# Kernel tuning notes

Hardware: AMD Instinct MI355X
Metric: run time of the kernel (lower is better)

Reference implementation:

```python
import jax, jax.numpy as jnp
import numpy as np

N_NODES = 100000
N_EDGES = 1600000
D_FEAT = 128
N_CLASSES = 10


def setup_inputs() -> dict:
    key = jax.random.key(0)
    ks = jax.random.split(key, 9)
    x = jax.random.normal(ks[0], (N_NODES, D_FEAT), dtype=jnp.float32)
    edge_src = jax.random.randint(ks[1], (N_EDGES,), 0, N_NODES, dtype=jnp.int32)
    edge_dst = jax.random.randint(ks[2], (N_EDGES,), 0, N_NODES, dtype=jnp.int32)
    s = 1.0 / np.sqrt(D_FEAT)
    W1 = jax.random.normal(ks[3], (D_FEAT, D_FEAT), dtype=jnp.float32) * s
    b1 = jax.random.normal(ks[4], (D_FEAT,), dtype=jnp.float32) * s
    W2 = jax.random.normal(ks[5], (D_FEAT, D_FEAT), dtype=jnp.float32) * s
    b2 = jax.random.normal(ks[6], (D_FEAT,), dtype=jnp.float32) * s
    W3 = jax.random.normal(ks[7], (D_FEAT, N_CLASSES), dtype=jnp.float32) * s
    b3 = jax.random.normal(ks[8], (N_CLASSES,), dtype=jnp.float32) * s
    return {"x": x, "edge_src": edge_src, "edge_dst": edge_dst,
            "W1": W1, "b1": b1, "W2": W2, "b2": b2, "W3": W3, "b3": b3}


def _neighbor_mean(x, src, dst, n_nodes):
    # scatter-mean of neighbor features; isolated nodes keep their own feature
    msg_sum = jax.ops.segment_sum(x[src], dst, num_segments=n_nodes)  # [N, D]
    deg = jax.ops.segment_sum(jnp.ones(src.shape, x.dtype), dst, num_segments=n_nodes)  # [N]
    mean = msg_sum / jnp.maximum(deg, 1.0)[:, None]
    return jnp.where(deg[:, None] > 0, mean, x)


def reference(x, edge_src, edge_dst, W1, b1, W2, b2, W3, b3):
    n = x.shape[0]
    # layer 1: aggregate -> linear -> tanh
    h = jnp.tanh(_neighbor_mean(x, edge_src, edge_dst, n) @ W1 + b1)
    # layer 2: aggregate -> linear -> tanh
    h = jnp.tanh(_neighbor_mean(h, edge_src, edge_dst, n) @ W2 + b2)
    # final linear head (no aggregation, no activation)
    logits = h @ W3 + b3
    return logits
```

## Files before the change

### kernel.cpp

```cpp
#include <hip/hip_runtime.h>

#define DF 128
#define AST 136
#define EPB 4096

typedef float f32x4 __attribute__((ext_vector_type(4)));
typedef short bf16x8 __attribute__((ext_vector_type(8)));

__device__ __forceinline__ ushort f2bf(float f) {
  union { float f; uint u; } c; c.f = f;
  uint u = c.u;
  uint r = (u + 0x7fffu + ((u >> 16) & 1u)) >> 16;
  return (ushort)r;
}
__device__ __forceinline__ float bf_lo(uint v) { union { uint u; float f; } c; c.u = v << 16; return c.f; }
__device__ __forceinline__ float bf_hi(uint v) { union { uint u; float f; } c; c.u = v & 0xffff0000u; return c.f; }

__device__ __forceinline__ void addv8(float* acc, uint4 v) {
  acc[0] += bf_lo(v.x); acc[1] += bf_hi(v.x);
  acc[2] += bf_lo(v.y); acc[3] += bf_hi(v.y);
  acc[4] += bf_lo(v.z); acc[5] += bf_hi(v.z);
  acc[6] += bf_lo(v.w); acc[7] += bf_hi(v.w);
}

__global__ void prep_hist_kernel(const int* __restrict__ dst, int* __restrict__ histG,
                                 int E, int nbuck, int nblocks,
                                 const float* __restrict__ x, ushort* __restrict__ xb,
                                 const float* __restrict__ W1, ushort* __restrict__ Wt1,
                                 const float* __restrict__ W2, ushort* __restrict__ Wt2,
                                 const float* __restrict__ W3, ushort* __restrict__ W3t,
                                 ushort* __restrict__ xbN, ushort* __restrict__ bufBN, int n4) {
  __shared__ int lh[512];
  int tid = threadIdx.x;
  if ((int)blockIdx.x < nblocks) {
    int blk = blockIdx.x;
    for (int i = tid; i < nbuck; i += 256) lh[i] = 0;
    __syncthreads();
    int base = blk * EPB + tid * 4;
#pragma unroll
    for (int it = 0; it < EPB / 1024; ++it) {
      int e = base + it * 1024;
      if (e + 3 < E) {
        int4 d4 = *(const int4*)(dst + e);
        atomicAdd(&lh[d4.x >> 8], 1);
        atomicAdd(&lh[d4.y >> 8], 1);
        atomicAdd(&lh[d4.z >> 8], 1);
        atomicAdd(&lh[d4.w >> 8], 1);
      } else {
#pragma unroll
        for (int q = 0; q < 4; ++q) {
          int ee = e + q;
          if (ee < E) atomicAdd(&lh[dst[ee] >> 8], 1);
        }
      }
    }
    __syncthreads();
    for (int i = tid; i < nbuck; i += 256) histG[(size_t)i * nblocks + blk] = lh[i];
    return;
  }
  int i = ((int)blockIdx.x - nblocks) * 256 + tid;
  if (i < n4) {
    float4 v = ((const float4*)x)[i];
    ushort4 o; o.x = f2bf(v.x); o.y = f2bf(v.y); o.z = f2bf(v.z); o.w = f2bf(v.w);
    ((ushort4*)xb)[i] = o;
    return;
  }
  int j = i - n4;
  if (j < DF * DF) {
    int nr = j >> 7, k = j & 127;
    Wt1[j] = f2bf(W1[(size_t)k * DF + nr]);
    return;
  }
  j -= DF * DF;
  if (j < DF * DF) {
    int nr = j >> 7, k = j & 127;
    Wt2[j] = f2bf(W2[(size_t)k * DF + nr]);
    return;
  }
  j -= DF * DF;
  if (j < 16 * DF) {
    int nr = j >> 7, k = j & 127;
    W3t[j] = (nr < 10) ? f2bf(W3[(size_t)k * 10 + nr]) : (ushort)0;
    return;
  }
  j -= 16 * DF;
  if (j < 16) { ((uint4*)xbN)[j] = (uint4){0, 0, 0, 0}; return; }
  j -= 16;
  if (j < 16) { ((uint4*)bufBN)[j] = (uint4){0, 0, 0, 0}; }
}

__global__ void scan1_kernel(const int* __restrict__ cnt, int* __restrict__ excl,
                             int* __restrict__ bsums, int n) {
  __shared__ int wsum[4];
  int t = threadIdx.x;
  int base = blockIdx.x * 1024 + t * 4;
  int v[4]; int s = 0;
#pragma unroll
  for (int i = 0; i < 4; i++) { int d = (base + i < n) ? cnt[base + i] : 0; v[i] = s; s += d; }
  int lane = t & 63, w = t >> 6;
  int sc = s;
#pragma unroll
  for (int off = 1; off < 64; off <<= 1) { int o = __shfl_up(sc, off); if (lane >= off) sc += o; }
  if (lane == 63) wsum[w] = sc;
  __syncthreads();
  int woff = 0;
  for (int i = 0; i < w; i++) woff += wsum[i];
  int toff = woff + (sc - s);
#pragma unroll
  for (int i = 0; i < 4; i++) if (base + i < n) excl[base + i] = toff + v[i];
  if (t == 255) bsums[blockIdx.x] = woff + sc;
}

__device__ __forceinline__ void scan_bsums_lds(const int* __restrict__ bsums, int nb,
                                               int* sbs, int* wsum) {
  int t = threadIdx.x;
  int v0 = (2 * t < nb) ? bsums[2 * t] : 0;
  int v1 = (2 * t + 1 < nb) ? bsums[2 * t + 1] : 0;
  int s = v0 + v1;
  int lane = t & 63, w = t >> 6;
  int sc = s;
#pragma unroll
  for (int off = 1; off < 64; off <<= 1) { int o = __shfl_up(sc, off); if (lane >= off) sc += o; }
  if (lane == 63) wsum[w] = sc;
  __syncthreads();
  int woff = 0;
  for (int i = 0; i < w; i++) woff += wsum[i];
  int excl = woff + sc - s;
  sbs[2 * t] = excl;
  sbs[2 * t + 1] = excl + v0;
  __syncthreads();
}

__global__ void bucket_scatter_kernel(const int* __restrict__ src, const int* __restrict__ dst,
                                      const int* __restrict__ histE, const int* __restrict__ bsums,
                                      int nb, uint* __restrict__ eb, int E, int nbuck, int nblocks) {
  __shared__ int lc[512];
  __shared__ int sbs[512];
  __shared__ int wsum[4];
  int tid = threadIdx.x, blk = blockIdx.x;
  scan_bsums_lds(bsums, nb, sbs, wsum);
  for (int i = tid; i < nbuck; i += 256) {
    int idx = i * nblocks + blk;
    lc[i] = histE[idx] + sbs[idx >> 10];
  }
  __syncthreads();
  int base = blk * EPB + tid * 4;
#pragma unroll
  for (int it = 0; it < EPB / 1024; ++it) {
    int e = base + it * 1024;
    if (e + 3 < E) {
      int4 s4 = *(const int4*)(src + e);
      int4 d4 = *(const int4*)(dst + e);
      int p0 = atomicAdd(&lc[d4.x >> 8], 1);
      eb[p0] = (uint)s4.x | ((uint)(d4.x & 255) << 24);
      int p1 = atomicAdd(&lc[d4.y >> 8], 1);
      eb[p1] = (uint)s4.y | ((uint)(d4.y & 255) << 24);
      int p2 = atomicAdd(&lc[d4.z >> 8], 1);
      eb[p2] = (uint)s4.z | ((uint)(d4.z & 255) << 24);
      int p3 = atomicAdd(&lc[d4.w >> 8], 1);
      eb[p3] = (uint)s4.w | ((uint)(d4.w & 255) << 24);
    } else {
#pragma unroll
      for (int q = 0; q < 4; ++q) {
        int ee = e + q;
        if (ee < E) {
          int d = dst[ee];
          int pos = atomicAdd(&lc[d >> 8], 1);
          eb[pos] = (uint)src[ee] | ((uint)(d & 255) << 24);
        }
      }
    }
  }
}

__global__ void bucket_sort_kernel(const uint* __restrict__ eb,
                                   const int* __restrict__ histE, const int* __restrict__ bsums,
                                   int nb, int* __restrict__ rowptr, int* __restrict__ csr,
                                   int N, int E, int nbuck, int nblocks) {
  __shared__ int cnt[256];
  __shared__ int cursor[256];
  __shared__ int sbs[512];
  __shared__ int wsum[4];
  int tid = threadIdx.x, b = blockIdx.x;
  scan_bsums_lds(bsums, nb, sbs, wsum);
  int idx = b * nblocks;
  int beg = histE[idx] + sbs[idx >> 10];
  int end = E;
  if (b + 1 < nbuck) { int i2 = (b + 1) * nblocks; end = histE[i2] + sbs[i2 >> 10]; }
  cnt[tid] = 0;
  __syncthreads();
  for (int e = beg + tid; e < end; e += 256)
    atomicAdd(&cnt[eb[e] >> 24], 1);
  __syncthreads();
  int v = cnt[tid];
  int lane = tid & 63, w = tid >> 6;
  int sc = v;
#pragma unroll
  for (int off = 1; off < 64; off <<= 1) { int o = __shfl_up(sc, off); if (lane >= off) sc += o; }
  if (lane == 63) wsum[w] = sc;
  __syncthreads();
  int woff = 0;
  for (int i = 0; i < w; i++) woff += wsum[i];
  int excl = woff + sc - v;
  int node = (b << 8) + tid;
  if (node <= N) rowptr[node] = beg + excl;
  cursor[tid] = beg + excl;
  __syncthreads();
  for (int e = beg + tid; e < end; e += 256) {
    uint vv = eb[e];
    int pos = atomicAdd(&cursor[vv >> 24], 1);
    csr[pos] = (int)(vv & 0x00FFFFFFu);
  }
}

__global__ __launch_bounds__(256) void aggregate_kernel(
    const ushort* __restrict__ xb, const int* __restrict__ rowptr,
    const int* __restrict__ csr, ushort* __restrict__ out, int n) {
  int tid = threadIdx.x;
  int node = (blockIdx.x * 256 + tid) >> 4;
  if (node >= n) return;
  uint c16 = (uint)(tid & 15) * 16u;
  int beg = rowptr[node], end = rowptr[node + 1];
  const char* xbase = (const char*)xb;
  float acc[8];
#pragma unroll
  for (int i = 0; i < 8; i++) acc[i] = 0.f;

#pragma unroll 1
  for (int e = beg; e < end; e += 4) {
    int e1 = e + 1, e2 = e + 2, e3 = e + 3;
    uint r0 = (uint)csr[e];
    uint r1 = (e1 < end) ? (uint)csr[e1] : (uint)n;
    uint r2 = (e2 < end) ? (uint)csr[e2] : (uint)n;
    uint r3 = (e3 < end) ? (uint)csr[e3] : (uint)n;
    uint4 v0 = *(const uint4*)(xbase + (r0 * 256u + c16));
    uint4 v1 = *(const uint4*)(xbase + (r1 * 256u + c16));
    uint4 v2 = *(const uint4*)(xbase + (r2 * 256u + c16));
    uint4 v3 = *(const uint4*)(xbase + (r3 * 256u + c16));
    addv8(acc, v0);
    addv8(acc, v1);
    addv8(acc, v2);
    addv8(acc, v3);
  }

  int deg = end - beg;
  uint4 r;
  if (deg > 0) {
    float inv = 1.0f / (float)deg;
    r.x = (uint)f2bf(acc[0] * inv) | ((uint)f2bf(acc[1] * inv) << 16);
    r.y = (uint)f2bf(acc[2] * inv) | ((uint)f2bf(acc[3] * inv) << 16);
    r.z = (uint)f2bf(acc[4] * inv) | ((uint)f2bf(acc[5] * inv) << 16);
    r.w = (uint)f2bf(acc[6] * inv) | ((uint)f2bf(acc[7] * inv) << 16);
  } else {
    r = *(const uint4*)(xbase + ((uint)node * 256u + c16));
  }
  *(uint4*)((char*)out + ((uint)node * 256u + c16)) = r;
}

__global__ __launch_bounds__(256) void gemm_tanh_mfma(
    const ushort* __restrict__ A, const ushort* __restrict__ Wt,
    const float* __restrict__ bias, ushort* __restrict__ out, int n, int ntiles) {
  __shared__ ushort Ws[128 * AST];
  __shared__ float bs[128];
  int tid = threadIdx.x;

  for (int i = tid; i < 128 * 16; i += 256) {
    int r = i >> 4, c = i & 15;
    uint4 v = ((const uint4*)(Wt + r * DF))[c];
    *(uint4*)&Ws[r * AST + c * 8] = v;
  }
  if (tid < 128) bs[tid] = bias[tid];
  __syncthreads();

  int lane = tid & 63, w = tid >> 6;
  int wr = (w >> 1) * 32;
  int wc = (w & 1) * 64;
  int r16 = lane & 15, g8 = (lane >> 4) * 8;

  for (int tile = blockIdx.x; tile < ntiles; tile += gridDim.x) {
    int node0 = tile * 64;
    int ra = node0 + wr + r16;      if (ra >= n) ra = n - 1;
    int rb = node0 + wr + 16 + r16; if (rb >= n) rb = n - 1;
    const ushort* pa = A + (size_t)ra * DF + g8;
    const ushort* pb = A + (size_t)rb * DF + g8;

    f32x4 acc[2][4];
#pragma unroll
    for (int i = 0; i < 2; i++)
#pragma unroll
      for (int j = 0; j < 4; j++) acc[i][j] = (f32x4){0.f, 0.f, 0.f, 0.f};

#pragma unroll
    for (int ks = 0; ks < 4; ++ks) {
      bf16x8 a0 = *(const bf16x8*)(pa + ks * 32);
      bf16x8 a1 = *(const bf16x8*)(pb + ks * 32);
      int k0 = ks * 32 + g8;
#pragma unroll
      for (int j = 0; j < 4; j++) {
        bf16x8 b = *(const bf16x8*)&Ws[(wc + j * 16 + r16) * AST + k0];
        acc[0][j] = __builtin_amdgcn_mfma_f32_16x16x32_bf16(a0, b, acc[0][j], 0, 0, 0);
        acc[1][j] = __builtin_amdgcn_mfma_f32_16x16x32_bf16(a1, b, acc[1][j], 0, 0, 0);
      }
    }

#pragma unroll
    for (int mi = 0; mi < 2; mi++) {
#pragma unroll
      for (int j = 0; j < 4; j++) {
        int col = wc + j * 16 + r16;
        float bv = bs[col];
        int rowb = wr + mi * 16 + (lane >> 4) * 4;
#pragma unroll
        for (int q = 0; q < 4; q++) {
          int node = node0 + rowb + q;
          if (node < n) {
            float vv = tanhf(acc[mi][j][q] + bv);
            out[(size_t)node * DF + col] = f2bf(vv);
          }
        }
      }
    }
  }
}

__global__ __launch_bounds__(256) void gemm2_head_mfma(
    const ushort* __restrict__ A, const ushort* __restrict__ Wt,
    const float* __restrict__ bias, const ushort* __restrict__ W3t,
    const float* __restrict__ b3, float* __restrict__ out, int n, int ntiles) {
  __shared__ ushort Hs[64 * AST];
  __shared__ ushort Ws[128 * AST];
  __shared__ ushort W3s[16 * AST];
  __shared__ float bs[128];
  int tid = threadIdx.x;

  for (int i = tid; i < 128 * 16; i += 256) {
    int r = i >> 4, c = i & 15;
    uint4 v = ((const uint4*)(Wt + r * DF))[c];
    *(uint4*)&Ws[r * AST + c * 8] = v;
  }
  {
    int r = tid >> 4, c = tid & 15;
    uint4 v = ((const uint4*)(W3t + r * DF))[c];
    *(uint4*)&W3s[r * AST + c * 8] = v;
  }
  if (tid < 128) bs[tid] = bias[tid];
  __syncthreads();

  int lane = tid & 63, w = tid >> 6;
  int wr = (w >> 1) * 32, wc = (w & 1) * 64;
  int r16 = lane & 15, g8 = (lane >> 4) * 8;

  for (int tile = blockIdx.x; tile < ntiles; tile += gridDim.x) {
    int node0 = tile * 64;
    int ra = node0 + wr + r16;      if (ra >= n) ra = n - 1;
    int rb = node0 + wr + 16 + r16; if (rb >= n) rb = n - 1;
    const ushort* pa = A + (size_t)ra * DF + g8;
    const ushort* pb = A + (size_t)rb * DF + g8;

    f32x4 acc[2][4];
#pragma unroll
    for (int i = 0; i < 2; i++)
#pragma unroll
      for (int j = 0; j < 4; j++) acc[i][j] = (f32x4){0.f, 0.f, 0.f, 0.f};

#pragma unroll
    for (int ks = 0; ks < 4; ++ks) {
      bf16x8 a0 = *(const bf16x8*)(pa + ks * 32);
      bf16x8 a1 = *(const bf16x8*)(pb + ks * 32);
      int k0 = ks * 32 + g8;
#pragma unroll
      for (int j = 0; j < 4; ++j) {
        bf16x8 b = *(const bf16x8*)&Ws[(wc + j * 16 + r16) * AST + k0];
        acc[0][j] = __builtin_amdgcn_mfma_f32_16x16x32_bf16(a0, b, acc[0][j], 0, 0, 0);
        acc[1][j] = __builtin_amdgcn_mfma_f32_16x16x32_bf16(a1, b, acc[1][j], 0, 0, 0);
      }
    }

    __syncthreads();
#pragma unroll
    for (int mi = 0; mi < 2; mi++) {
#pragma unroll
      for (int j = 0; j < 4; j++) {
        int col = wc + j * 16 + r16;
        float bv = bs[col];
        int rowb = wr + mi * 16 + (lane >> 4) * 4;
#pragma unroll
        for (int q = 0; q < 4; q++)
          Hs[(rowb + q) * AST + col] = f2bf(tanhf(acc[mi][j][q] + bv));
      }
    }
    __syncthreads();

    f32x4 h = (f32x4){0.f, 0.f, 0.f, 0.f};
#pragma unroll
    for (int ks = 0; ks < 4; ++ks) {
      int k0 = ks * 32 + g8;
      bf16x8 a = *(const bf16x8*)&Hs[(w * 16 + r16) * AST + k0];
      bf16x8 b = *(const bf16x8*)&W3s[r16 * AST + k0];
      h = __builtin_amdgcn_mfma_f32_16x16x32_bf16(a, b, h, 0, 0, 0);
    }
    if (r16 < 10) {
      float bv = b3[r16];
      int rowb = w * 16 + (lane >> 4) * 4;
#pragma unroll
      for (int q = 0; q < 4; q++) {
        int node = node0 + rowb + q;
        if (node < n) out[(size_t)node * 10 + r16] = h[q] + bv;
      }
    }
  }
}

extern "C" void kernel_launch(void* const* d_in, const int* in_sizes, int n_in,
                              void* d_out, int out_size, void* d_ws, size_t ws_size,
                              hipStream_t stream) {
  const float* x    = (const float*)d_in[0];
  const int*   esrc = (const int*)d_in[1];
  const int*   edst = (const int*)d_in[2];
  const float* W1   = (const float*)d_in[3];
  const float* b1   = (const float*)d_in[4];
  const float* W2   = (const float*)d_in[5];
  const float* b2   = (const float*)d_in[6];
  const float* W3   = (const float*)d_in[7];
  const float* b3   = (const float*)d_in[8];
  float* out = (float*)d_out;

  const int N = in_sizes[0] / DF;
  const int E = in_sizes[1];

  const int nbuck   = (N + 255) >> 8;
  const int nblocks = (E + EPB - 1) / EPB;
  const int M = nbuck * nblocks;

  char* ws = (char*)d_ws;
  int*  rowptr = (int*)ws;
  int*  csr    = rowptr + (N + 1);
  int*  histG  = csr + E;
  int*  histE  = histG + M;
  int*  bsums2 = histE + M;
  uint* eb     = (uint*)(bsums2 + 1024);
  size_t off = (size_t)((char*)(eb + E) - ws);
  off = (off + 255) & ~(size_t)255;
  ushort* xb  = (ushort*)(ws + off);     off += (size_t)(N + 1) * DF * 2; off = (off + 255) & ~(size_t)255;
  ushort* Wt1 = (ushort*)(ws + off);     off += (size_t)DF * DF * 2;
  ushort* Wt2 = (ushort*)(ws + off);     off += (size_t)DF * DF * 2;
  ushort* W3t = (ushort*)(ws + off);     off += (size_t)16 * DF * 2; off = (off + 255) & ~(size_t)255;
  ushort* bufA = (ushort*)(ws + off);    off += (size_t)N * DF * 2; off = (off + 255) & ~(size_t)255;
  ushort* bufB = (ushort*)(ws + off);

  int n4 = N * DF / 4;
  int prep_total = n4 + 2 * DF * DF + 16 * DF + 32;
  int prep_blocks = (prep_total + 255) / 256;
  prep_hist_kernel<<<nblocks + prep_blocks, 256, 0, stream>>>(
      edst, histG, E, nbuck, nblocks,
      x, xb, W1, Wt1, W2, Wt2, W3, W3t,
      xb + (size_t)N * DF, bufB + (size_t)N * DF, n4);

  int nb_m = (M + 1023) / 1024;
  scan1_kernel<<<nb_m, 256, 0, stream>>>(histG, histE, bsums2, M);
  bucket_scatter_kernel<<<nblocks, 256, 0, stream>>>(esrc, edst, histE, bsums2, nb_m, eb, E, nbuck, nblocks);
  bucket_sort_kernel<<<nbuck, 256, 0, stream>>>(eb, histE, bsums2, nb_m, rowptr, csr, N, E, nbuck, nblocks);

  int agg_blocks = (N + 15) / 16;
  int ntiles = (N + 63) / 64;
  int gemm_grid = ntiles < 512 ? ntiles : 512;

  aggregate_kernel<<<agg_blocks, 256, 0, stream>>>(xb, rowptr, csr, bufA, N);
  gemm_tanh_mfma<<<gemm_grid, 256, 0, stream>>>(bufA, Wt1, b1, bufB, N, ntiles);
  aggregate_kernel<<<agg_blocks, 256, 0, stream>>>(bufB, rowptr, csr, bufA, N);
  gemm2_head_mfma<<<gemm_grid, 256, 0, stream>>>(bufA, Wt2, b2, W3t, b3, out, N, ntiles);
}
```

Before: 204.4 us.

## Apply weights before aggregation, overlap first GEMM with scan, fuse head

The code uses linearity to swap the order of mean-aggregation and the linear layer, since mean(x)@W equals mean(x@W). That lets the first GEMM run on the raw features, so it is folded into the scan kernel and overlaps with CSR construction. Bias and tanh now run in the aggregation kernels, and the 10-class head is computed in the second aggregation using shuffle reductions. This removes one GEMM epilogue pass and the separate head kernel. In exchange, the bf16 rounding now happens at a different point, and head arithmetic moves from MFMA to scalar FMAs.

Measured after the change: 197.4 us. -3.4%, faster.

```diff
diff --git a/kernel.cpp b/kernel.cpp
--- a/kernel.cpp
+++ b/kernel.cpp
@@ -28,8 +28,7 @@
                                  const float* __restrict__ x, ushort* __restrict__ xb,
                                  const float* __restrict__ W1, ushort* __restrict__ Wt1,
                                  const float* __restrict__ W2, ushort* __restrict__ Wt2,
-                                 const float* __restrict__ W3, ushort* __restrict__ W3t,
-                                 ushort* __restrict__ xbN, ushort* __restrict__ bufBN, int n4) {
+                                 ushort* __restrict__ zbN, ushort* __restrict__ ybN, int n4) {
   __shared__ int lh[512];
   int tid = threadIdx.x;
   if ((int)blockIdx.x < nblocks) {
@@ -78,37 +77,107 @@
     return;
   }
   j -= DF * DF;
-  if (j < 16 * DF) {
-    int nr = j >> 7, k = j & 127;
-    W3t[j] = (nr < 10) ? f2bf(W3[(size_t)k * 10 + nr]) : (ushort)0;
-    return;
-  }
-  j -= 16 * DF;
-  if (j < 16) { ((uint4*)xbN)[j] = (uint4){0, 0, 0, 0}; return; }
+  if (j < 16) { ((uint4*)zbN)[j] = (uint4){0, 0, 0, 0}; return; }
   j -= 16;
-  if (j < 16) { ((uint4*)bufBN)[j] = (uint4){0, 0, 0, 0}; }
-}
-
-__global__ void scan1_kernel(const int* __restrict__ cnt, int* __restrict__ excl,
-                             int* __restrict__ bsums, int n) {
+  if (j < 16) { ((uint4*)ybN)[j] = (uint4){0, 0, 0, 0}; }
+}
+
+__device__ __forceinline__ void gemm_tiles(const ushort* __restrict__ A,
+                                           const ushort* __restrict__ Ws,
+                                           ushort* __restrict__ out, int n, int ntiles,
+                                           int tile0, int tstride, int tid) {
+  int lane = tid & 63, w = tid >> 6;
+  int wr = (w >> 1) * 32, wc = (w & 1) * 64;
+  int r16 = lane & 15, g8 = (lane >> 4) * 8;
+  for (int tile = tile0; tile < ntiles; tile += tstride) {
+    int node0 = tile * 64;
+    int ra = node0 + wr + r16;      if (ra >= n) ra = n - 1;
+    int rb = node0 + wr + 16 + r16; if (rb >= n) rb = n - 1;
+    const ushort* pa = A + (size_t)ra * DF + g8;
+    const ushort* pb = A + (size_t)rb * DF + g8;
+
+    f32x4 acc[2][4];
+#pragma unroll
+    for (int i = 0; i < 2; i++)
+#pragma unroll
+      for (int j = 0; j < 4; j++) acc[i][j] = (f32x4){0.f, 0.f, 0.f, 0.f};
+
+#pragma unroll
+    for (int ks = 0; ks < 4; ++ks) {
+      bf16x8 a0 = *(const bf16x8*)(pa + ks * 32);
+      bf16x8 a1 = *(const bf16x8*)(pb + ks * 32);
+      int k0 = ks * 32 + g8;
+#pragma unroll
+      for (int j = 0; j < 4; j++) {
+        bf16x8 b = *(const bf16x8*)&Ws[(wc + j * 16 + r16) * AST + k0];
+        acc[0][j] = __builtin_amdgcn_mfma_f32_16x16x32_bf16(a0, b, acc[0][j], 0, 0, 0);
+        acc[1][j] = __builtin_amdgcn_mfma_f32_16x16x32_bf16(a1, b, acc[1][j], 0, 0, 0);
+      }
+    }
+
+#pragma unroll
+    for (int mi = 0; mi < 2; mi++) {
+#pragma unroll
+      for (int j = 0; j < 4; j++) {
+        int col = wc + j * 16 + r16;
+        int rowb = wr + mi * 16 + (lane >> 4) * 4;
+#pragma unroll
+        for (int q = 0; q < 4; q++) {
+          int node = node0 + rowb + q;
+          if (node < n) out[(size_t)node * DF + col] = f2bf(acc[mi][j][q]);
+        }
+      }
+    }
+  }
+}
+
+__global__ __launch_bounds__(256) void scan1_gemm_kernel(
+    const int* __restrict__ cnt, int* __restrict__ excl, int* __restrict__ bsums, int Mn,
+    int nb_m, const ushort* __restrict__ xb, const ushort* __restrict__ Wt1,
+    ushort* __restrict__ yb, int n, int ntiles) {
+  __shared__ ushort Ws[128 * AST];
   __shared__ int wsum[4];
   int t = threadIdx.x;
-  int base = blockIdx.x * 1024 + t * 4;
-  int v[4]; int s = 0;
-#pragma unroll
-  for (int i = 0; i < 4; i++) { int d = (base + i < n) ? cnt[base + i] : 0; v[i] = s; s += d; }
-  int lane = t & 63, w = t >> 6;
-  int sc = s;
-#pragma unroll
-  for (int off = 1; off < 64; off <<= 1) { int o = __shfl_up(sc, off); if (lane >= off) sc += o; }
-  if (lane == 63) wsum[w] = sc;
-  __syncthreads();
-  int woff = 0;
-  for (int i = 0; i < w; i++) woff += wsum[i];
-  int toff = woff + (sc - s);
-#pragma unroll
-  for (int i = 0; i < 4; i++) if (base + i < n) excl[base + i] = toff + v[i];
-  if (t == 255) bsums[blockIdx.x] = woff + sc;
+  if ((int)blockIdx.x < nb_m) {
+    int base = blockIdx.x * 1024 + t * 4;
+    int v[4]; int s = 0;
+#pragma unroll
+    for (int i = 0; i < 4; i++) { int d = (base + i < Mn) ? cnt[base + i] : 0; v[i] = s; s += d; }
+    int lane = t & 63, w = t >> 6;
+    int sc = s;
+#pragma unroll
+    for (int off = 1; off < 64; off <<= 1) { int o = __shfl_up(sc, off); if (lane >= off) sc += o; }
+    if (lane == 63) wsum[w] = sc;
+    __syncthreads();
+    int woff = 0;
+    for (int i = 0; i < w; i++) woff += wsum[i];
+    int toff = woff + (sc - s);
+#pragma unroll
+    for (int i = 0; i < 4; i++) if (base + i < Mn) excl[base + i] = toff + v[i];
+    if (t == 255) bsums[blockIdx.x] = woff + sc;
+    return;
+  }
+  for (int i = t; i < 128 * 16; i += 256) {
+    int r = i >> 4, c = i & 15;
+    uint4 v = ((const uint4*)(Wt1 + r * DF))[c];
+    *(uint4*)&Ws[r * AST + c * 8] = v;
+  }
+  __syncthreads();
+  gemm_tiles(xb, Ws, yb, n, ntiles, (int)blockIdx.x - nb_m, (int)gridDim.x - nb_m, t);
+}
+
+__global__ __launch_bounds__(256) void gemm_plain_kernel(
+    const ushort* __restrict__ A, const ushort* __restrict__ Wt,
+    ushort* __restrict__ out, int n, int ntiles) {
+  __shared__ ushort Ws[128 * AST];
+  int t = threadIdx.x;
+  for (int i = t; i < 128 * 16; i += 256) {
+    int r = i >> 4, c = i & 15;
+    uint4 v = ((const uint4*)(Wt + r * DF))[c];
+    *(uint4*)&Ws[r * AST + c * 8] = v;
+  }
+  __syncthreads();
+  gemm_tiles(A, Ws, out, n, ntiles, blockIdx.x, gridDim.x, t);
 }
 
 __device__ __forceinline__ void scan_bsums_lds(const int* __restrict__ bsums, int nb,
@@ -213,202 +282,111 @@
   }
 }
 
-__global__ __launch_bounds__(256) void aggregate_kernel(
-    const ushort* __restrict__ xb, const int* __restrict__ rowptr,
-    const int* __restrict__ csr, ushort* __restrict__ out, int n) {
+__device__ __forceinline__ void gather_mean(const ushort* __restrict__ src,
+                                            const int* __restrict__ rowptr,
+                                            const int* __restrict__ csr,
+                                            int node, int n, uint c16, float* acc) {
+  int beg = rowptr[node], end = rowptr[node + 1];
+  const char* xbase = (const char*)src;
+#pragma unroll
+  for (int i = 0; i < 8; i++) acc[i] = 0.f;
+  int deg = end - beg;
+  if (deg > 0) {
+#pragma unroll 1
+    for (int e = beg; e < end; e += 4) {
+      int e1 = e + 1, e2 = e + 2, e3 = e + 3;
+      uint r0 = (uint)csr[e];
+      uint r1 = (e1 < end) ? (uint)csr[e1] : (uint)n;
+      uint r2 = (e2 < end) ? (uint)csr[e2] : (uint)n;
+      uint r3 = (e3 < end) ? (uint)csr[e3] : (uint)n;
+      uint4 v0 = *(const uint4*)(xbase + (r0 * 256u + c16));
+      uint4 v1 = *(const uint4*)(xbase + (r1 * 256u + c16));
+      uint4 v2 = *(const uint4*)(xbase + (r2 * 256u + c16));
+      uint4 v3 = *(const uint4*)(xbase + (r3 * 256u + c16));
+      addv8(acc, v0);
+      addv8(acc, v1);
+      addv8(acc, v2);
+      addv8(acc, v3);
+    }
+    float inv = 1.0f / (float)deg;
+#pragma unroll
+    for (int i = 0; i < 8; i++) acc[i] *= inv;
+  } else {
+    uint4 v = *(const uint4*)(xbase + ((uint)node * 256u + c16));
+    float t[8] = {0, 0, 0, 0, 0, 0, 0, 0};
+    addv8(t, v);
+#pragma unroll
+    for (int i = 0; i < 8; i++) acc[i] = t[i];
+  }
+}
+
+__global__ __launch_bounds__(256) void agg_bias_tanh_kernel(
+    const ushort* __restrict__ yb, const int* __restrict__ rowptr,
+    const int* __restrict__ csr, const float* __restrict__ bias,
+    ushort* __restrict__ h1, int n) {
   int tid = threadIdx.x;
   int node = (blockIdx.x * 256 + tid) >> 4;
   if (node >= n) return;
   uint c16 = (uint)(tid & 15) * 16u;
-  int beg = rowptr[node], end = rowptr[node + 1];
-  const char* xbase = (const char*)xb;
   float acc[8];
-#pragma unroll
-  for (int i = 0; i < 8; i++) acc[i] = 0.f;
-
-#pragma unroll 1
-  for (int e = beg; e < end; e += 4) {
-    int e1 = e + 1, e2 = e + 2, e3 = e + 3;
-    uint r0 = (uint)csr[e];
-    uint r1 = (e1 < end) ? (uint)csr[e1] : (uint)n;
-    uint r2 = (e2 < end) ? (uint)csr[e2] : (uint)n;
-    uint r3 = (e3 < end) ? (uint)csr[e3] : (uint)n;
-    uint4 v0 = *(const uint4*)(xbase + (r0 * 256u + c16));
-    uint4 v1 = *(const uint4*)(xbase + (r1 * 256u + c16));
-    uint4 v2 = *(const uint4*)(xbase + (r2 * 256u + c16));
-    uint4 v3 = *(const uint4*)(xbase + (r3 * 256u + c16));
-    addv8(acc, v0);
-    addv8(acc, v1);
-    addv8(acc, v2);
-    addv8(acc, v3);
-  }
-
-  int deg = end - beg;
+  gather_mean(yb, rowptr, csr, node, n, c16, acc);
+  int d8 = (tid & 15) * 8;
+  float4 bA = *(const float4*)(bias + d8);
+  float4 bB = *(const float4*)(bias + d8 + 4);
+  float h0 = tanhf(acc[0] + bA.x), hh1 = tanhf(acc[1] + bA.y);
+  float h2 = tanhf(acc[2] + bA.z), h3 = tanhf(acc[3] + bA.w);
+  float h4 = tanhf(acc[4] + bB.x), h5 = tanhf(acc[5] + bB.y);
+  float h6 = tanhf(acc[6] + bB.z), h7 = tanhf(acc[7] + bB.w);
   uint4 r;
-  if (deg > 0) {
-    float inv = 1.0f / (float)deg;
-    r.x = (uint)f2bf(acc[0] * inv) | ((uint)f2bf(acc[1] * inv) << 16);
-    r.y = (uint)f2bf(acc[2] * inv) | ((uint)f2bf(acc[3] * inv) << 16);
-    r.z = (uint)f2bf(acc[4] * inv) | ((uint)f2bf(acc[5] * inv) << 16);
-    r.w = (uint)f2bf(acc[6] * inv) | ((uint)f2bf(acc[7] * inv) << 16);
-  } else {
-    r = *(const uint4*)(xbase + ((uint)node * 256u + c16));
-  }
-  *(uint4*)((char*)out + ((uint)node * 256u + c16)) = r;
-}
-
-__global__ __launch_bounds__(256) void gemm_tanh_mfma(
-    const ushort* __restrict__ A, const ushort* __restrict__ Wt,
-    const float* __restrict__ bias, ushort* __restrict__ out, int n, int ntiles) {
-  __shared__ ushort Ws[128 * AST];
-  __shared__ float bs[128];
+  r.x = (uint)f2bf(h0) | ((uint)f2bf(hh1) << 16);
+  r.y = (uint)f2bf(h2) | ((uint)f2bf(h3) << 16);
+  r.z = (uint)f2bf(h4) | ((uint)f2bf(h5) << 16);
+  r.w = (uint)f2bf(h6) | ((uint)f2bf(h7) << 16);
+  *(uint4*)((char*)h1 + ((uint)node * 256u + c16)) = r;
+}
+
+__global__ __launch_bounds__(256) void agg_head_kernel(
+    const ushort* __restrict__ zb, const int* __restrict__ rowptr,
+    const int* __restrict__ csr, const float* __restrict__ b2,
+    const float* __restrict__ W3, const float* __restrict__ b3,
+    float* __restrict__ out, int n) {
+  __shared__ float W3s[DF * 10];
   int tid = threadIdx.x;
-
-  for (int i = tid; i < 128 * 16; i += 256) {
-    int r = i >> 4, c = i & 15;
-    uint4 v = ((const uint4*)(Wt + r * DF))[c];
-    *(uint4*)&Ws[r * AST + c * 8] = v;
-  }
-  if (tid < 128) bs[tid] = bias[tid];
-  __syncthreads();
-
-  int lane = tid & 63, w = tid >> 6;
-  int wr = (w >> 1) * 32;
-  int wc = (w & 1) * 64;
-  int r16 = lane & 15, g8 = (lane >> 4) * 8;
-
-  for (int tile = blockIdx.x; tile < ntiles; tile += gridDim.x) {
-    int node0 = tile * 64;
-    int ra = node0 + wr + r16;      if (ra >= n) ra = n - 1;
-    int rb = node0 + wr + 16 + r16; if (rb >= n) rb = n - 1;
-    const ushort* pa = A + (size_t)ra * DF + g8;
-    const ushort* pb = A + (size_t)rb * DF + g8;
-
-    f32x4 acc[2][4];
-#pragma unroll
-    for (int i = 0; i < 2; i++)
-#pragma unroll
-      for (int j = 0; j < 4; j++) acc[i][j] = (f32x4){0.f, 0.f, 0.f, 0.f};
-
-#pragma unroll
-    for (int ks = 0; ks < 4; ++ks) {
-      bf16x8 a0 = *(const bf16x8*)(pa + ks * 32);
-      bf16x8 a1 = *(const bf16x8*)(pb + ks * 32);
-      int k0 = ks * 32 + g8;
-#pragma unroll
-      for (int j = 0; j < 4; j++) {
-        bf16x8 b = *(const bf16x8*)&Ws[(wc + j * 16 + r16) * AST + k0];
-        acc[0][j] = __builtin_amdgcn_mfma_f32_16x16x32_bf16(a0, b, acc[0][j], 0, 0, 0);
-        acc[1][j] = __builtin_amdgcn_mfma_f32_16x16x32_bf16(a1, b, acc[1][j], 0, 0, 0);
-      }
-    }
-
-#pragma unroll
-    for (int mi = 0; mi < 2; mi++) {
-#pragma unroll
-      for (int j = 0; j < 4; j++) {
-        int col = wc + j * 16 + r16;
-        float bv = bs[col];
-        int rowb = wr + mi * 16 + (lane >> 4) * 4;
-#pragma unroll
-        for (int q = 0; q < 4; q++) {
-          int node = node0 + rowb + q;
-          if (node < n) {
-            float vv = tanhf(acc[mi][j][q] + bv);
-            out[(size_t)node * DF + col] = f2bf(vv);
-          }
-        }
-      }
-    }
-  }
-}
-
-__global__ __launch_bounds__(256) void gemm2_head_mfma(
-    const ushort* __restrict__ A, const ushort* __restrict__ Wt,
-    const float* __restrict__ bias, const ushort* __restrict__ W3t,
-    const float* __restrict__ b3, float* __restrict__ out, int n, int ntiles) {
-  __shared__ ushort Hs[64 * AST];
-  __shared__ ushort Ws[128 * AST];
-  __shared__ ushort W3s[16 * AST];
-  __shared__ float bs[128];
-  int tid = threadIdx.x;
-
-  for (int i = tid; i < 128 * 16; i += 256) {
-    int r = i >> 4, c = i & 15;
-    uint4 v = ((const uint4*)(Wt + r * DF))[c];
-    *(uint4*)&Ws[r * AST + c * 8] = v;
-  }
-  {
-    int r = tid >> 4, c = tid & 15;
-    uint4 v = ((const uint4*)(W3t + r * DF))[c];
-    *(uint4*)&W3s[r * AST + c * 8] = v;
-  }
-  if (tid < 128) bs[tid] = bias[tid];
-  __syncthreads();
-
-  int lane = tid & 63, w = tid >> 6;
-  int wr = (w >> 1) * 32, wc = (w & 1) * 64;
-  int r16 = lane & 15, g8 = (lane >> 4) * 8;
-
-  for (int tile = blockIdx.x; tile < ntiles; tile += gridDim.x) {
-    int node0 = tile * 64;
-    int ra = node0 + wr + r16;      if (ra >= n) ra = n - 1;
-    int rb = node0 + wr + 16 + r16; if (rb >= n) rb = n - 1;
-    const ushort* pa = A + (size_t)ra * DF + g8;
-    const ushort* pb = A + (size_t)rb * DF + g8;
-
-    f32x4 acc[2][4];
-#pragma unroll
-    for (int i = 0; i < 2; i++)
-#pragma unroll
-      for (int j = 0; j < 4; j++) acc[i][j] = (f32x4){0.f, 0.f, 0.f, 0.f};
-
-#pragma unroll
-    for (int ks = 0; ks < 4; ++ks) {
-      bf16x8 a0 = *(const bf16x8*)(pa + ks * 32);
-      bf16x8 a1 = *(const bf16x8*)(pb + ks * 32);
-      int k0 = ks * 32 + g8;
-#pragma unroll
-      for (int j = 0; j < 4; ++j) {
-        bf16x8 b = *(const bf16x8*)&Ws[(wc + j * 16 + r16) * AST + k0];
-        acc[0][j] = __builtin_amdgcn_mfma_f32_16x16x32_bf16(a0, b, acc[0][j], 0, 0, 0);
-        acc[1][j] = __builtin_amdgcn_mfma_f32_16x16x32_bf16(a1, b, acc[1][j], 0, 0, 0);
-      }
-    }
-
-    __syncthreads();
-#pragma unroll
-    for (int mi = 0; mi < 2; mi++) {
-#pragma unroll
-      for (int j = 0; j < 4; j++) {
-        int col = wc + j * 16 + r16;
-        float bv = bs[col];
-        int rowb = wr + mi * 16 + (lane >> 4) * 4;
-#pragma unroll
-        for (int q = 0; q < 4; q++)
-          Hs[(rowb + q) * AST + col] = f2bf(tanhf(acc[mi][j][q] + bv));
-      }
-    }
-    __syncthreads();
-
-    f32x4 h = (f32x4){0.f, 0.f, 0.f, 0.f};
-#pragma unroll
-    for (int ks = 0; ks < 4; ++ks) {
-      int k0 = ks * 32 + g8;
-      bf16x8 a = *(const bf16x8*)&Hs[(w * 16 + r16) * AST + k0];
-      bf16x8 b = *(const bf16x8*)&W3s[r16 * AST + k0];
-      h = __builtin_amdgcn_mfma_f32_16x16x32_bf16(a, b, h, 0, 0, 0);
-    }
-    if (r16 < 10) {
-      float bv = b3[r16];
-      int rowb = w * 16 + (lane >> 4) * 4;
-#pragma unroll
-      for (int q = 0; q < 4; q++) {
-        int node = node0 + rowb + q;
-        if (node < n) out[(size_t)node * 10 + r16] = h[q] + bv;
-      }
-    }
-  }
+  for (int i = tid; i < DF * 10; i += 256) W3s[i] = W3[i];
+  __syncthreads();
+  int node = (blockIdx.x * 256 + tid) >> 4;
+  if (node >= n) return;
+  uint c16 = (uint)(tid & 15) * 16u;
+  float acc[8];
+  gather_mean(zb, rowptr, csr, node, n, c16, acc);
+  int d8 = (tid & 15) * 8;
+  float4 bA = *(const float4*)(b2 + d8);
+  float4 bB = *(const float4*)(b2 + d8 + 4);
+  float h[8];
+  h[0] = tanhf(acc[0] + bA.x); h[1] = tanhf(acc[1] + bA.y);
+  h[2] = tanhf(acc[2] + bA.z); h[3] = tanhf(acc[3] + bA.w);
+  h[4] = tanhf(acc[4] + bB.x); h[5] = tanhf(acc[5] + bB.y);
+  h[6] = tanhf(acc[6] + bB.z); h[7] = tanhf(acc[7] + bB.w);
+  float part[10];
+#pragma unroll
+  for (int j = 0; j < 10; j++) part[j] = 0.f;
+#pragma unroll
+  for (int i = 0; i < 8; i++) {
+    const float* wrow = &W3s[(d8 + i) * 10];
+#pragma unroll
+    for (int j = 0; j < 10; j++) part[j] += h[i] * wrow[j];
+  }
+#pragma unroll
+  for (int j = 0; j < 10; j++) {
+    part[j] += __shfl_xor(part[j], 1);
+    part[j] += __shfl_xor(part[j], 2);
+    part[j] += __shfl_xor(part[j], 4);
+    part[j] += __shfl_xor(part[j], 8);
+  }
+  int l16 = tid & 15;
+#pragma unroll
+  for (int j = 0; j < 10; j++)
+    if (l16 == j) out[(size_t)node * 10 + j] = part[j] + b3[j];
 }
 
 extern "C" void kernel_launch(void* const* d_in, const int* in_sizes, int n_in,
@@ -443,30 +421,31 @@
   off = (off + 255) & ~(size_t)255;
   ushort* xb  = (ushort*)(ws + off);     off += (size_t)(N + 1) * DF * 2; off = (off + 255) & ~(size_t)255;
   ushort* Wt1 = (ushort*)(ws + off);     off += (size_t)DF * DF * 2;
-  ushort* Wt2 = (ushort*)(ws + off);     off += (size_t)DF * DF * 2;
-  ushort* W3t = (ushort*)(ws + off);     off += (size_t)16 * DF * 2; off = (off + 255) & ~(size_t)255;
-  ushort* bufA = (ushort*)(ws + off);    off += (size_t)N * DF * 2; off = (off + 255) & ~(size_t)255;
-  ushort* bufB = (ushort*)(ws + off);
+  ushort* Wt2 = (ushort*)(ws + off);     off += (size_t)DF * DF * 2; off = (off + 255) & ~(size_t)255;
+  ushort* yb  = (ushort*)(ws + off);     off += (size_t)(N + 1) * DF * 2; off = (off + 255) & ~(size_t)255;
+  ushort* h1  = (ushort*)(ws + off);
+  ushort* zb  = xb;
 
   int n4 = N * DF / 4;
-  int prep_total = n4 + 2 * DF * DF + 16 * DF + 32;
+  int prep_total = n4 + 2 * DF * DF + 32;
   int prep_blocks = (prep_total + 255) / 256;
   prep_hist_kernel<<<nblocks + prep_blocks, 256, 0, stream>>>(
       edst, histG, E, nbuck, nblocks,
-      x, xb, W1, Wt1, W2, Wt2, W3, W3t,
-      xb + (size_t)N * DF, bufB + (size_t)N * DF, n4);
+      x, xb, W1, Wt1, W2, Wt2,
+      xb + (size_t)N * DF, yb + (size_t)N * DF, n4);
 
   int nb_m = (M + 1023) / 1024;
-  scan1_kernel<<<nb_m, 256, 0, stream>>>(histG, histE, bsums2, M);
+  int ntiles = (N + 63) / 64;
+
+  scan1_gemm_kernel<<<nb_m + 512, 256, 0, stream>>>(
+      histG, histE, bsums2, M, nb_m, xb, Wt1, yb, N, ntiles);
+
   bucket_scatter_kernel<<<nblocks, 256, 0, stream>>>(esrc, edst, histE, bsums2, nb_m, eb, E, nbuck, nblocks);
   bucket_sort_kernel<<<nbuck, 256, 0, stream>>>(eb, histE, bsums2, nb_m, rowptr, csr, N, E, nbuck, nblocks);
 
   int agg_blocks = (N + 15) / 16;
-  int ntiles = (N + 63) / 64;
-  int gemm_grid = ntiles < 512 ? ntiles : 512;
-
-  aggregate_kernel<<<agg_blocks, 256, 0, stream>>>(xb, rowptr, csr, bufA, N);
-  gemm_tanh_mfma<<<gemm_grid, 256, 0, stream>>>(bufA, Wt1, b1, bufB, N, ntiles);
-  aggregate_kernel<<<agg_blocks, 256, 0, stream>>>(bufB, rowptr, csr, bufA, N);
-  gemm2_head_mfma<<<gemm_grid, 256, 0, stream>>>(bufA, Wt2, b2, W3t, b3, out, N, ntiles);
-}
+
+  agg_bias_tanh_kernel<<<agg_blocks, 256, 0, stream>>>(yb, rowptr, csr, b1, h1, N);
+  gemm_plain_kernel<<<512, 256, 0, stream>>>(h1, Wt2, zb, N, ntiles);
+  agg_head_kernel<<<agg_blocks, 256, 0, stream>>>(zb, rowptr, csr, b2, W3, b3, out, N);
+}
```
